# Optimization experiments

Hardware: AMD Instinct MI355X
Metric: run time of the kernel (lower is better)

## Reference

```python
import jax, jax.numpy as jnp
import numpy as np

NUM_HEADS = 12
HEAD_DIM = 64
EPS = 1e-6


def _layernorm(x, g, b):
    mu = jnp.mean(x, axis=-1, keepdims=True)
    var = jnp.mean(jnp.square(x - mu), axis=-1, keepdims=True)
    return (x - mu) * jax.lax.rsqrt(var + EPS) * g + b


def setup_inputs() -> dict:
    key = jax.random.key(0)
    ks = jax.random.split(key, 8)
    D, DFF = 768, 3072
    s = lambda d: 1.0 / np.sqrt(d)
    return {
        "hidden_states": jax.random.normal(ks[0], (4, 2048, D), jnp.float32),
        "ln1_g": jnp.ones((D,), jnp.float32),
        "ln1_b": jnp.zeros((D,), jnp.float32),
        "w_qkv": jax.random.normal(ks[1], (D, 3 * D), jnp.float32) * s(D),
        "b_qkv": jnp.zeros((3 * D,), jnp.float32),
        "w_attn": jax.random.normal(ks[2], (D, D), jnp.float32) * s(D),
        "b_attn": jnp.zeros((D,), jnp.float32),
        "ln2_g": jnp.ones((D,), jnp.float32),
        "ln2_b": jnp.zeros((D,), jnp.float32),
        "w_in": jax.random.normal(ks[3], (D, DFF), jnp.float32) * s(D),
        "b_in": jnp.zeros((DFF,), jnp.float32),
        "w_out": jax.random.normal(ks[4], (DFF, D), jnp.float32) * s(DFF),
        "b_out": jnp.zeros((D,), jnp.float32),
    }


def reference(hidden_states, ln1_g, ln1_b, w_qkv, b_qkv, w_attn, b_attn,
              ln2_g, ln2_b, w_in, b_in, w_out, b_out):
    B, S, D = hidden_states.shape
    residual = hidden_states
    h = _layernorm(hidden_states, ln1_g, ln1_b)
    # QKV: [B,S,3D] -> [B,S,3,H,hd] -> [3,B,H,S,hd]
    qkv = (h @ w_qkv + b_qkv).reshape(B, S, 3, NUM_HEADS, HEAD_DIM)
    qkv = jnp.transpose(qkv, (2, 0, 3, 1, 4))
    scale = HEAD_DIM ** (-0.5)
    q, k, v = qkv[0] * scale, qkv[1], qkv[2]
    scores = jnp.einsum("bhqd,bhkd->bhqk", q, k)
    attn = jax.nn.softmax(scores, axis=-1)
    o = jnp.einsum("bhqk,bhkd->bhqd", attn, v)
    o = jnp.transpose(o, (0, 2, 1, 3)).reshape(B, S, D)
    h = residual + (o @ w_attn + b_attn)
    residual2 = h
    h2 = _layernorm(h, ln2_g, ln2_b)
    h2 = jax.nn.gelu(h2 @ w_in + b_in, approximate=False)
    h2 = h2 @ w_out + b_out
    return residual2 + h2
```

## Files before the change

### kernel.cpp

```cpp
#include <hip/hip_runtime.h>

typedef __bf16 bf16_t;
typedef bf16_t bf16x8 __attribute__((ext_vector_type(8)));
typedef float f32x4 __attribute__((ext_vector_type(4)));
typedef unsigned short ushortx8 __attribute__((ext_vector_type(8)));
typedef unsigned short ushortx4 __attribute__((ext_vector_type(4)));
typedef short short4v __attribute__((ext_vector_type(4)));

union U8 { ushortx4 h[2]; bf16x8 b; ushortx8 u; };
union SV { bf16_t h[4]; short4v s; };

__device__ __forceinline__ unsigned short f2bf(float f) {
  union { bf16_t h; unsigned short u; } cv;
  cv.h = (bf16_t)f;
  return cv.u;
}

__device__ __forceinline__ void gl_lds16(const unsigned short* g, unsigned short* l) {
  __builtin_amdgcn_global_load_lds((const __attribute__((address_space(1))) void*)g,
                                   (__attribute__((address_space(3))) void*)l,
                                   16, 0, 0);
}

__device__ __forceinline__ float gelu_fast(float v) {
  float v3 = v * v * v;
  float z = -2.30211886f * v - 0.102945f * v3;
  float e = exp2f(z);
  return v * __builtin_amdgcn_rcpf(1.0f + e);
}

__global__ __launch_bounds__(256) void ln_kernel(const float* __restrict__ x,
                                                 const float* __restrict__ g,
                                                 const float* __restrict__ b,
                                                 unsigned short* __restrict__ out) {
  int row = blockIdx.x;
  int t = threadIdx.x;
  const float* xr = x + (size_t)row * 768;
  float v0 = xr[t], v1 = xr[t + 256], v2 = xr[t + 512];
  __shared__ float red[4];
  float s = v0 + v1 + v2;
  for (int o = 32; o > 0; o >>= 1) s += __shfl_down(s, o, 64);
  if ((t & 63) == 0) red[t >> 6] = s;
  __syncthreads();
  float mu = (red[0] + red[1] + red[2] + red[3]) * (1.0f / 768.0f);
  __syncthreads();
  float d0 = v0 - mu, d1 = v1 - mu, d2 = v2 - mu;
  s = d0 * d0 + d1 * d1 + d2 * d2;
  for (int o = 32; o > 0; o >>= 1) s += __shfl_down(s, o, 64);
  if ((t & 63) == 0) red[t >> 6] = s;
  __syncthreads();
  float var = (red[0] + red[1] + red[2] + red[3]) * (1.0f / 768.0f);
  float rs = rsqrtf(var + 1e-6f);
  unsigned short* orow = out + (size_t)row * 768;
  orow[t]       = f2bf(d0 * rs * g[t]       + b[t]);
  orow[t + 256] = f2bf(d1 * rs * g[t + 256] + b[t + 256]);
  orow[t + 512] = f2bf(d2 * rs * g[t + 512] + b[t + 512]);
}

__global__ __launch_bounds__(256) void transpose_all(
    const float* __restrict__ w_qkv, const float* __restrict__ w_attn,
    const float* __restrict__ w_in, const float* __restrict__ w_out,
    unsigned short* __restrict__ wqkvT, unsigned short* __restrict__ wattnT,
    unsigned short* __restrict__ winT, unsigned short* __restrict__ woutT) {
  int id = blockIdx.x;
  const float* W; unsigned short* WT; int K, N, nx, ny;
  if (id < 1728)      { W = w_qkv;  WT = wqkvT;  K = 768;  N = 2304; nx = id % 72; ny = id / 72; }
  else if (id < 2304) { id -= 1728; W = w_attn; WT = wattnT; K = 768;  N = 768;  nx = id % 24; ny = id / 24; }
  else if (id < 4608) { id -= 2304; W = w_in;   WT = winT;   K = 768;  N = 3072; nx = id % 96; ny = id / 96; }
  else                { id -= 4608; W = w_out;  WT = woutT;  K = 3072; N = 768;  nx = id % 24; ny = id / 24; }
  __shared__ float tile[32][33];
  int n0 = nx * 32, k0 = ny * 32;
  int tx = threadIdx.x, ty = threadIdx.y;
  for (int i = 0; i < 4; i++)
    tile[ty + i * 8][tx] = W[(size_t)(k0 + ty + i * 8) * N + n0 + tx];
  __syncthreads();
  for (int i = 0; i < 4; i++)
    WT[(size_t)(n0 + ty + i * 8) * K + k0 + tx] = f2bf(tile[tx][ty + i * 8]);
}

template <int EPI, int TM>
__device__ __forceinline__ void gemm_body(const unsigned short* __restrict__ A,
                                          const unsigned short* __restrict__ BT,
                                          const float* __restrict__ bias,
                                          const float* resid,
                                          void* out, unsigned short* vt, int os,
                                          int N, int K) {
  constexpr int MI = TM / 32;
  constexpr int ASZ = TM * 32;
  __shared__ __align__(16) unsigned short smem[2 * ASZ + 8192];

  int t = threadIdx.x;
  int w = t >> 6, lane = t & 63, ln = lane & 15, quad = lane >> 4;
  int wm = w & 1, wn = w >> 1;
  int m0 = blockIdx.y * TM, n0 = blockIdx.x * 128;

  int srow = w * 16 + (lane >> 2);
  int scol = (lane & 3) * 8;
  const unsigned short* gA0 = A + (size_t)(m0 + srow) * K + scol;
  const unsigned short* gA1 = gA0 + (size_t)64 * K;
  const unsigned short* gB0 = BT + (size_t)(n0 + srow) * K + scol;
  const unsigned short* gB1 = gB0 + (size_t)64 * K;

  auto stage = [&](int buf) {
    unsigned short* Ab = smem + buf * ASZ;
    unsigned short* Bb = smem + 2 * ASZ + buf * 4096;
    gl_lds16(gA0, Ab + w * 512);
    if constexpr (TM == 128) gl_lds16(gA1, Ab + 2048 + w * 512);
    gl_lds16(gB0, Bb + w * 512);
    gl_lds16(gB1, Bb + 2048 + w * 512);
    gA0 += 32; gA1 += 32; gB0 += 32; gB1 += 32;
  };

  f32x4 acc[MI][4];
  f32x4 zero = {0.f, 0.f, 0.f, 0.f};
  for (int mi = 0; mi < MI; mi++)
    for (int ni = 0; ni < 4; ni++) acc[mi][ni] = zero;

  int nk = K >> 5;
  stage(0);
  int cur = 0;
  for (int kt = 0; kt < nk; kt++) {
    __syncthreads();
    if (kt + 1 < nk) stage(cur ^ 1);
    const unsigned short* Ac = smem + cur * ASZ;
    const unsigned short* Bc = smem + 2 * ASZ + cur * 4096;
    bf16x8 af[MI], bfr[4];
    for (int mi = 0; mi < MI; mi++)
      af[mi] = *(const bf16x8*)&Ac[(wm * (TM / 2) + mi * 16 + ln) * 32 + quad * 8];
    for (int ni = 0; ni < 4; ni++)
      bfr[ni] = *(const bf16x8*)&Bc[(wn * 64 + ni * 16 + ln) * 32 + quad * 8];
    for (int mi = 0; mi < MI; mi++)
      for (int ni = 0; ni < 4; ni++)
        acc[mi][ni] = __builtin_amdgcn_mfma_f32_16x16x32_bf16(af[mi], bfr[ni],
                                                              acc[mi][ni], 0, 0, 0);
    cur ^= 1;
  }

  if (EPI == 2) {
    float* outp = (float*)out;
    for (int mi = 0; mi < MI; mi++) {
      for (int ni = 0; ni < 4; ni++) {
        int col = n0 + wn * 64 + ni * 16 + ln;
        float bv = bias[col];
        for (int r = 0; r < 4; r++) {
          int row = m0 + wm * (TM / 2) + mi * 16 + quad * 4 + r;
          float v = acc[mi][ni][r] + bv;
          v += resid[(size_t)row * N + col];
          outp[(size_t)row * N + col] = v;
        }
      }
    }
  } else {
    __syncthreads();
    unsigned short* Cs16 = smem + w * 1024;
    unsigned short* outp = (unsigned short*)out;
    for (int mi = 0; mi < MI; mi++) {
      for (int ni = 0; ni < 4; ni++) {
        int col = n0 + wn * 64 + ni * 16 + ln;
        float bv = bias[col];
        for (int r = 0; r < 4; r++) {
          float v = acc[mi][ni][r] + bv;
          if (EPI == 0) {
            if (col < 768) v *= 0.18033688f;
          } else {
            v = gelu_fast(v);
          }
          Cs16[(quad * 4 + r) * 64 + ni * 16 + ln] = f2bf(v);
        }
      }
      __syncthreads();
      if (EPI == 0 && n0 >= 1536) {
        int c = n0 - 1536 + wn * 64 + lane;
        int s0 = m0 + wm * (TM / 2) + mi * 16;
        int bb = s0 >> 11, sl = s0 & 2047;
        ushortx8 lo, hi;
        for (int r = 0; r < 8; r++) lo[r] = Cs16[r * 64 + lane];
        for (int r = 0; r < 8; r++) hi[r] = Cs16[(8 + r) * 64 + lane];
        size_t vbase = ((size_t)(bb * 768 + c)) * 2048 + sl;
        *(ushortx8*)&vt[vbase] = lo;
        *(ushortx8*)&vt[vbase + 8] = hi;
      } else {
        int OS = (EPI == 0) ? os : N;
        for (int j = 0; j < 2; j++) {
          int rrow = j * 8 + (lane >> 3);
          int ch = (lane & 7) * 8;
          ushortx8 pv = *(const ushortx8*)&Cs16[rrow * 64 + ch];
          *(ushortx8*)&outp[(size_t)(m0 + wm * (TM / 2) + mi * 16 + rrow) * OS +
                            n0 + wn * 64 + ch] = pv;
        }
      }
      __syncthreads();
    }
  }
}

__global__ __launch_bounds__(256) void gemm_qkv(const unsigned short* A,
    const unsigned short* BT, const float* bias, void* out, unsigned short* vt,
    int N, int K) {
  gemm_body<0, 128>(A, BT, bias, nullptr, out, vt, 1536, N, K);
}
__global__ __launch_bounds__(256) void gemm_attnout(const unsigned short* A,
    const unsigned short* BT, const float* bias, const float* resid, void* out,
    int N, int K) {
  gemm_body<2, 64>(A, BT, bias, resid, out, nullptr, N, N, K);
}
__global__ __launch_bounds__(256) void gemm_ffn1(const unsigned short* A,
    const unsigned short* BT, const float* bias, void* out, int N, int K) {
  gemm_body<1, 128>(A, BT, bias, nullptr, out, nullptr, N, N, K);
}
__global__ __launch_bounds__(256) void gemm_ffn2(const unsigned short* A,
    const unsigned short* BT, const float* bias, const float* resid, void* out,
    int N, int K) {
  gemm_body<2, 64>(A, BT, bias, resid, out, nullptr, N, N, K);
}

__global__ __launch_bounds__(512, 4) void flash_attn(
    const unsigned short* __restrict__ qk, const unsigned short* __restrict__ v_t,
    unsigned short* __restrict__ o) {
  int qt = blockIdx.x;
  int bh = blockIdx.y;
  int b = bh / 12, h = bh % 12;
  int t = threadIdx.x;
  int w = t >> 6, lane = t & 63, ln = lane & 15, quad = lane >> 4;
  int qg = w & 3, kh2 = w >> 2;

  __shared__ __align__(16) unsigned short smem[18432];
  int qrow0 = b * 2048 + qt * 128;
  int qw = qrow0 + qg * 32;

  bf16x8 qf[2][2];
  for (int qi = 0; qi < 2; qi++)
    for (int kh = 0; kh < 2; kh++)
      qf[qi][kh] = *(const bf16x8*)&qk[(size_t)(qw + qi * 16 + ln) * 1536 +
                                      h * 64 + kh * 32 + quad * 8];

  SV ones;
  for (int r = 0; r < 4; r++) ones.h[r] = (bf16_t)1.0f;

  f32x4 zero = {0.f, 0.f, 0.f, 0.f};
  f32x4 o_acc[4][2];
  for (int df = 0; df < 4; df++)
    for (int qi = 0; qi < 2; qi++) o_acc[df][qi] = zero;
  f32x4 l_acc[2] = {zero, zero};

  int sr = t >> 3, sc = (t & 7) * 8;
  ushortx8 kreg = *(const ushortx8*)&qk[(size_t)(b * 2048 + sr) * 1536 + 768 + h * 64 + sc];
  ushortx8 vreg = *(const ushortx8*)&v_t[(size_t)(bh * 64 + sr) * 2048 + sc];

  for (int kt = 0; kt < 32; kt++) {
    unsigned short* Ks = smem + (kt & 1) * 9216;
    unsigned short* Vt = Ks + 4608;
    *(ushortx8*)&Ks[sr * 72 + sc] = kreg;
    *(ushortx8*)&Vt[sr * 72 + sc] = vreg;
    __syncthreads();
    if (kt < 31) {
      int krow0 = b * 2048 + (kt + 1) * 64;
      kreg = *(const ushortx8*)&qk[(size_t)(krow0 + sr) * 1536 + 768 + h * 64 + sc];
      vreg = *(const ushortx8*)&v_t[(size_t)(bh * 64 + sr) * 2048 + (kt + 1) * 64 + sc];
    }

    for (int kf = 0; kf < 2; kf++) {
      int krow = kh2 * 32 + kf * 16;
      f32x4 ST[2] = {zero, zero};
      bf16x8 kA0 = *(const bf16x8*)&Ks[(krow + ln) * 72 + quad * 8];
      bf16x8 kA1 = *(const bf16x8*)&Ks[(krow + ln) * 72 + 32 + quad * 8];
      __builtin_amdgcn_s_setprio(1);
      for (int qi = 0; qi < 2; qi++) {
        ST[qi] = __builtin_amdgcn_mfma_f32_16x16x32_bf16(kA0, qf[qi][0], ST[qi], 0, 0, 0);
        ST[qi] = __builtin_amdgcn_mfma_f32_16x16x32_bf16(kA1, qf[qi][1], ST[qi], 0, 0, 0);
      }
      __builtin_amdgcn_s_setprio(0);
      short4v pT[2];
      for (int qi = 0; qi < 2; qi++) {
        SV pv;
        for (int r = 0; r < 4; r++)
          pv.h[r] = (bf16_t)__builtin_amdgcn_exp2f(ST[qi][r]);
        pT[qi] = pv.s;
      }
      __builtin_amdgcn_s_setprio(1);
      for (int qi = 0; qi < 2; qi++)
        l_acc[qi] = __builtin_amdgcn_mfma_f32_16x16x16bf16_1k(
            ones.s, pT[qi], l_acc[qi], 0, 0, 0);
      for (int df = 0; df < 4; df++) {
        short4v vA = *(const short4v*)&Vt[(df * 16 + ln) * 72 + krow + quad * 4];
        for (int qi = 0; qi < 2; qi++)
          o_acc[df][qi] = __builtin_amdgcn_mfma_f32_16x16x16bf16_1k(
              vA, pT[qi], o_acc[df][qi], 0, 0, 0);
      }
      __builtin_amdgcn_s_setprio(0);
    }
  }

  __syncthreads();
  float* fb = (float*)smem;
  float* fbl = fb + 8320;
  if (kh2 == 1) {
    for (int df = 0; df < 4; df++)
      for (int qi = 0; qi < 2; qi++)
        for (int r = 0; r < 4; r++)
          fb[qg * 2080 + (qi * 16 + ln) * 65 + df * 16 + quad * 4 + r] =
              o_acc[df][qi][r];
    if (quad == 0)
      for (int qi = 0; qi < 2; qi++)
        fbl[qg * 32 + qi * 16 + ln] = l_acc[qi][0];
  }
  __syncthreads();
  float inv[2];
  if (kh2 == 0) {
    for (int qi = 0; qi < 2; qi++) {
      float lt = l_acc[qi][0] + fbl[qg * 32 + qi * 16 + ln];
      inv[qi] = __builtin_amdgcn_rcpf(lt);
    }
    for (int df = 0; df < 4; df++)
      for (int qi = 0; qi < 2; qi++)
        for (int r = 0; r < 4; r++)
          o_acc[df][qi][r] += fb[qg * 2080 + (qi * 16 + ln) * 65 + df * 16 + quad * 4 + r];
  }
  __syncthreads();
  if (kh2 == 0) {
    unsigned short* Osm = smem + qg * 2304;
    for (int qi = 0; qi < 2; qi++)
      for (int df = 0; df < 4; df++)
        for (int r = 0; r < 4; r++)
          Osm[(qi * 16 + ln) * 72 + df * 16 + quad * 4 + r] =
              f2bf(o_acc[df][qi][r] * inv[qi]);
  }
  __syncthreads();
  if (kh2 == 0) {
    unsigned short* Osm = smem + qg * 2304;
    for (int p2 = 0; p2 < 4; p2++) {
      int rr = p2 * 8 + (lane >> 3);
      int ch = (lane & 7) * 8;
      ushortx8 u = *(const ushortx8*)&Osm[rr * 72 + ch];
      *(ushortx8*)&o[(size_t)(qw + rr) * 768 + h * 64 + ch] = u;
    }
  }
}

extern "C" void kernel_launch(void* const* d_in, const int* in_sizes, int n_in,
                              void* d_out, int out_size, void* d_ws, size_t ws_size,
                              hipStream_t stream) {
  const float* hidden = (const float*)d_in[0];
  const float* ln1_g  = (const float*)d_in[1];
  const float* ln1_b  = (const float*)d_in[2];
  const float* w_qkv  = (const float*)d_in[3];
  const float* b_qkv  = (const float*)d_in[4];
  const float* w_attn = (const float*)d_in[5];
  const float* b_attn = (const float*)d_in[6];
  const float* ln2_g  = (const float*)d_in[7];
  const float* ln2_b  = (const float*)d_in[8];
  const float* w_in   = (const float*)d_in[9];
  const float* b_in   = (const float*)d_in[10];
  const float* w_out  = (const float*)d_in[11];
  const float* b_out  = (const float*)d_in[12];
  float* out = (float*)d_out;

  char* ws = (char*)d_ws;
  unsigned short* wqkvT  = (unsigned short*)(ws + 0);
  unsigned short* wattnT = (unsigned short*)(ws + 3538944);
  unsigned short* winT   = (unsigned short*)(ws + 4718592);
  unsigned short* woutT  = (unsigned short*)(ws + 9437184);
  unsigned short* bufX   = (unsigned short*)(ws + 14155776);
  unsigned short* bufBig = (unsigned short*)(ws + 26738688);
  unsigned short* bufQK  = bufBig;
  unsigned short* v_t    = (unsigned short*)(ws + 26738688 + 25165824);

  transpose_all<<<6912, dim3(32, 8), 0, stream>>>(w_qkv, w_attn, w_in, w_out,
                                                  wqkvT, wattnT, winT, woutT);
  ln_kernel<<<8192, 256, 0, stream>>>(hidden, ln1_g, ln1_b, bufX);
  gemm_qkv<<<dim3(18, 64), 256, 0, stream>>>(bufX, wqkvT, b_qkv, (void*)bufQK,
                                             v_t, 2304, 768);
  flash_attn<<<dim3(16, 48), 512, 0, stream>>>(bufQK, v_t, bufX);
  gemm_attnout<<<dim3(6, 128), 256, 0, stream>>>(bufX, wattnT, b_attn, hidden,
                                                 (void*)out, 768, 768);
  ln_kernel<<<8192, 256, 0, stream>>>(out, ln2_g, ln2_b, bufX);
  gemm_ffn1<<<dim3(24, 64), 256, 0, stream>>>(bufX, winT, b_in, (void*)bufBig,
                                              3072, 768);
  gemm_ffn2<<<dim3(6, 128), 256, 0, stream>>>(bufBig, woutT, b_out, out,
                                              (void*)out, 768, 3072);
}
```

Before: 409.3 us.

## Add BK template with XOR-swizzled LDS, XCD-aware block remap for GEMMs and attention

Makes the GEMM K-tile depth a template parameter, using BK=64 for the two residual-epilogue GEMMs (64-row tiles) and keeping 32 for the others. LDS tiles get an XOR swizzle on the 16-byte slot index to cut bank conflicts in the MFMA operand reads. Block indices for the GEMMs and flash attention are remapped so that consecutive workgroups, which are dealt round-robin across the 8 XCDs, share nearby tiles and reuse L2. This adds more LDS per block for the BK=64 kernels, which may reduce occupancy.

```diff
diff --git a/kernel.cpp b/kernel.cpp
--- a/kernel.cpp
+++ b/kernel.cpp
@@ -78,7 +78,7 @@
     WT[(size_t)(n0 + ty + i * 8) * K + k0 + tx] = f2bf(tile[tx][ty + i * 8]);
 }
 
-template <int EPI, int TM>
+template <int EPI, int TM, int BK>
 __device__ __forceinline__ void gemm_body(const unsigned short* __restrict__ A,
                                           const unsigned short* __restrict__ BT,
                                           const float* __restrict__ bias,
@@ -86,29 +86,50 @@
                                           void* out, unsigned short* vt, int os,
                                           int N, int K) {
   constexpr int MI = TM / 32;
-  constexpr int ASZ = TM * 32;
-  __shared__ __align__(16) unsigned short smem[2 * ASZ + 8192];
+  constexpr int ASZ = TM * BK;
+  constexpr int BSZ = 128 * BK;
+  constexpr int RP = 512 / BK;
+  constexpr int NA = TM / (4 * RP);
+  constexpr int NB = 128 / (4 * RP);
+  constexpr int SM = BK / 8 - 1;
+  __shared__ __align__(16) unsigned short smem[2 * (ASZ + BSZ)];
 
   int t = threadIdx.x;
   int w = t >> 6, lane = t & 63, ln = lane & 15, quad = lane >> 4;
   int wm = w & 1, wn = w >> 1;
-  int m0 = blockIdx.y * TM, n0 = blockIdx.x * 128;
-
-  int srow = w * 16 + (lane >> 2);
-  int scol = (lane & 3) * 8;
-  const unsigned short* gA0 = A + (size_t)(m0 + srow) * K + scol;
-  const unsigned short* gA1 = gA0 + (size_t)64 * K;
-  const unsigned short* gB0 = BT + (size_t)(n0 + srow) * K + scol;
-  const unsigned short* gB1 = gB0 + (size_t)64 * K;
+
+  int gx = gridDim.x;
+  int nwg = gx * gridDim.y;
+  int flat = blockIdx.y * gx + blockIdx.x;
+  int nf = (flat & 7) * (nwg >> 3) + (flat >> 3);
+  int m0 = (nf / gx) * TM, n0 = (nf % gx) * 128;
+
+  int lrow = lane / (BK / 8);
+  int lslot = lane % (BK / 8);
+  int scol = ((lslot ^ (lrow & SM)) * 8);
+
+  const unsigned short* gA[NA];
+  const unsigned short* gB[NB];
+#pragma unroll
+  for (int i = 0; i < NA; i++)
+    gA[i] = A + (size_t)(m0 + (i * 4 + w) * RP + lrow) * K + scol;
+#pragma unroll
+  for (int i = 0; i < NB; i++)
+    gB[i] = BT + (size_t)(n0 + (i * 4 + w) * RP + lrow) * K + scol;
 
   auto stage = [&](int buf) {
     unsigned short* Ab = smem + buf * ASZ;
-    unsigned short* Bb = smem + 2 * ASZ + buf * 4096;
-    gl_lds16(gA0, Ab + w * 512);
-    if constexpr (TM == 128) gl_lds16(gA1, Ab + 2048 + w * 512);
-    gl_lds16(gB0, Bb + w * 512);
-    gl_lds16(gB1, Bb + 2048 + w * 512);
-    gA0 += 32; gA1 += 32; gB0 += 32; gB1 += 32;
+    unsigned short* Bb = smem + 2 * ASZ + buf * BSZ;
+#pragma unroll
+    for (int i = 0; i < NA; i++) {
+      gl_lds16(gA[i], Ab + (i * 4 + w) * 512);
+      gA[i] += BK;
+    }
+#pragma unroll
+    for (int i = 0; i < NB; i++) {
+      gl_lds16(gB[i], Bb + (i * 4 + w) * 512);
+      gB[i] += BK;
+    }
   };
 
   f32x4 acc[MI][4];
@@ -116,23 +137,34 @@
   for (int mi = 0; mi < MI; mi++)
     for (int ni = 0; ni < 4; ni++) acc[mi][ni] = zero;
 
-  int nk = K >> 5;
+  int nk = K / BK;
   stage(0);
   int cur = 0;
   for (int kt = 0; kt < nk; kt++) {
     __syncthreads();
     if (kt + 1 < nk) stage(cur ^ 1);
     const unsigned short* Ac = smem + cur * ASZ;
-    const unsigned short* Bc = smem + 2 * ASZ + cur * 4096;
-    bf16x8 af[MI], bfr[4];
-    for (int mi = 0; mi < MI; mi++)
-      af[mi] = *(const bf16x8*)&Ac[(wm * (TM / 2) + mi * 16 + ln) * 32 + quad * 8];
-    for (int ni = 0; ni < 4; ni++)
-      bfr[ni] = *(const bf16x8*)&Bc[(wn * 64 + ni * 16 + ln) * 32 + quad * 8];
-    for (int mi = 0; mi < MI; mi++)
-      for (int ni = 0; ni < 4; ni++)
-        acc[mi][ni] = __builtin_amdgcn_mfma_f32_16x16x32_bf16(af[mi], bfr[ni],
-                                                              acc[mi][ni], 0, 0, 0);
+    const unsigned short* Bc = smem + 2 * ASZ + cur * BSZ;
+#pragma unroll
+    for (int ks = 0; ks < BK / 32; ks++) {
+      bf16x8 af[MI], bfr[4];
+#pragma unroll
+      for (int mi = 0; mi < MI; mi++) {
+        int r = wm * (TM / 2) + mi * 16 + ln;
+        af[mi] = *(const bf16x8*)&Ac[r * BK + (((ks * 4 + quad) ^ (r & SM)) * 8)];
+      }
+#pragma unroll
+      for (int ni = 0; ni < 4; ni++) {
+        int r = wn * 64 + ni * 16 + ln;
+        bfr[ni] = *(const bf16x8*)&Bc[r * BK + (((ks * 4 + quad) ^ (r & SM)) * 8)];
+      }
+#pragma unroll
+      for (int mi = 0; mi < MI; mi++)
+#pragma unroll
+        for (int ni = 0; ni < 4; ni++)
+          acc[mi][ni] = __builtin_amdgcn_mfma_f32_16x16x32_bf16(af[mi], bfr[ni],
+                                                                acc[mi][ni], 0, 0, 0);
+    }
     cur ^= 1;
   }
 
@@ -197,28 +229,30 @@
 __global__ __launch_bounds__(256) void gemm_qkv(const unsigned short* A,
     const unsigned short* BT, const float* bias, void* out, unsigned short* vt,
     int N, int K) {
-  gemm_body<0, 128>(A, BT, bias, nullptr, out, vt, 1536, N, K);
+  gemm_body<0, 128, 32>(A, BT, bias, nullptr, out, vt, 1536, N, K);
 }
 __global__ __launch_bounds__(256) void gemm_attnout(const unsigned short* A,
     const unsigned short* BT, const float* bias, const float* resid, void* out,
     int N, int K) {
-  gemm_body<2, 64>(A, BT, bias, resid, out, nullptr, N, N, K);
+  gemm_body<2, 64, 64>(A, BT, bias, resid, out, nullptr, N, N, K);
 }
 __global__ __launch_bounds__(256) void gemm_ffn1(const unsigned short* A,
     const unsigned short* BT, const float* bias, void* out, int N, int K) {
-  gemm_body<1, 128>(A, BT, bias, nullptr, out, nullptr, N, N, K);
+  gemm_body<1, 128, 32>(A, BT, bias, nullptr, out, nullptr, N, N, K);
 }
 __global__ __launch_bounds__(256) void gemm_ffn2(const unsigned short* A,
     const unsigned short* BT, const float* bias, const float* resid, void* out,
     int N, int K) {
-  gemm_body<2, 64>(A, BT, bias, resid, out, nullptr, N, N, K);
+  gemm_body<2, 64, 64>(A, BT, bias, resid, out, nullptr, N, N, K);
 }
 
 __global__ __launch_bounds__(512, 4) void flash_attn(
     const unsigned short* __restrict__ qk, const unsigned short* __restrict__ v_t,
     unsigned short* __restrict__ o) {
-  int qt = blockIdx.x;
-  int bh = blockIdx.y;
+  int flat = blockIdx.y * 16 + blockIdx.x;
+  int nf = (flat & 7) * 96 + (flat >> 3);
+  int qt = nf % 16;
+  int bh = nf / 16;
   int b = bh / 12, h = bh % 12;
   int t = threadIdx.x;
   int w = t >> 6, lane = t & 63, ln = lane & 15, quad = lane >> 4;
```

Measured after the change: 393.4 us. 3.9% less time.
